# Kernel tuning notes

Hardware: AMD Instinct MI355X
Metric: run time of the kernel (lower is better)

The kernel has to match this reference:

```python
import jax, jax.numpy as jnp
import numpy as np

B_, T_, N_ = 32, 96, 68
IN_F, HID, GRU_H, NCLS = 3, 128, 128, 10
DEG = 8
N_NODES = B_ * T_ * N_
N_EDGES = N_NODES * DEG


def setup_inputs() -> dict:
    key = jax.random.key(0)
    ks = jax.random.split(key, 16)
    s = 0.05
    rn = lambda k, shp: (jax.random.normal(k, shp, jnp.float32) * s)
    return {
        "x": jax.random.normal(ks[0], (N_NODES, IN_F), jnp.float32),
        "edge_index": jax.random.randint(ks[1], (2, N_EDGES), 0, N_NODES, jnp.int32),
        "W_gcn0": rn(ks[2], (IN_F, HID)),
        "b_gcn0": jnp.zeros((HID,), jnp.float32),
        "W_gcn1": rn(ks[3], (HID, HID)),
        "b_gcn1": jnp.zeros((HID,), jnp.float32),
        "W_mlp": rn(ks[4], (HID, HID)),
        "b_mlp": jnp.zeros((HID,), jnp.float32),
        "W_ih": rn(ks[5], (3 * GRU_H, HID)),
        "W_hh": rn(ks[6], (3 * GRU_H, GRU_H)),
        "b_ih": jnp.zeros((3 * GRU_H,), jnp.float32),
        "b_hh": jnp.zeros((3 * GRU_H,), jnp.float32),
        "W_c1": rn(ks[7], (GRU_H, GRU_H // 2)),
        "b_c1": jnp.zeros((GRU_H // 2,), jnp.float32),
        "W_c2": rn(ks[8], (GRU_H // 2, NCLS)),
        "b_c2": jnp.zeros((NCLS,), jnp.float32),
        "B": B_, "T": T_, "N": N_,
    }


def reference(x, edge_index, W_gcn0, b_gcn0, W_gcn1, b_gcn1, W_mlp, b_mlp,
              W_ih, W_hh, b_ih, b_hh, W_c1, b_c1, W_c2, b_c2, B, T, N):
    n_nodes = x.shape[0]
    src, dst = edge_index[0], edge_index[1]
    # GCN degree with self-loops: deg[i] = 1 + in-degree(i)
    deg = jnp.ones((n_nodes,), x.dtype).at[dst].add(1.0)
    d_isqrt = jax.lax.rsqrt(deg)
    self_norm = (d_isqrt * d_isqrt)[:, None]  # self-loop norm = 1/deg
    edge_norm = (d_isqrt[src] * d_isqrt[dst])[:, None]

    def gcn(h, W, b):
        h = h @ W
        agg = jax.ops.segment_sum(h[src] * edge_norm, dst, num_segments=n_nodes)
        return agg + h * self_norm + b

    h = jax.nn.relu(gcn(x, W_gcn0, b_gcn0))
    h = jax.nn.relu(gcn(h, W_gcn1, b_gcn1))
    h = jax.nn.relu(h @ W_mlp + b_mlp)  # node_mlp (dropout off in eval)

    frames = h.reshape(B, T, N, -1).mean(axis=2)  # [B, T, HID] frame pooling

    def gru_step(hs, xt):
        gi = xt @ W_ih.T + b_ih
        gh = hs @ W_hh.T + b_hh
        ir, iz, inn = jnp.split(gi, 3, axis=-1)
        hr, hz, hn = jnp.split(gh, 3, axis=-1)
        r = jax.nn.sigmoid(ir + hr)
        z = jax.nn.sigmoid(iz + hz)
        n_new = jnp.tanh(inn + r * hn)
        return (1.0 - z) * n_new + z * hs, None

    h0 = jnp.zeros((B, GRU_H), frames.dtype)
    hT, _ = jax.lax.scan(gru_step, h0, jnp.swapaxes(frames, 0, 1))

    hidden = jax.nn.relu(hT @ W_c1 + b_c1)
    return hidden @ W_c2 + b_c2  # logits [B, num_classes]
```

## Files before the change

kernel.cpp:

```cpp
#include <hip/hip_runtime.h>

#define NN_TOT 208896
#define E_TOT  1671168
#define B_SZ   32
#define T_SZ   96
#define NPF    68
#define HID    128
#define NBINS  204
#define CAP    9216
#define NSB    816

typedef _Float16 f16x8 __attribute__((ext_vector_type(8)));
typedef _Float16 f16x2v __attribute__((ext_vector_type(2)));
typedef float f32x4 __attribute__((ext_vector_type(4)));

__global__ __launch_bounds__(256) void k_scatter(const int* __restrict__ src, const int* __restrict__ dst,
                                                 int* __restrict__ gcur, int* __restrict__ er_tmp,
                                                 const float* __restrict__ Wih, const float* __restrict__ Whh,
                                                 const float* __restrict__ W1, const float* __restrict__ Wm,
                                                 const float* __restrict__ W0, const float* __restrict__ b0,
                                                 _Float16* __restrict__ Wihh, _Float16* __restrict__ Wihl,
                                                 _Float16* __restrict__ W1p, _Float16* __restrict__ Wmp,
                                                 _Float16* __restrict__ Whhp, _Float16* __restrict__ W0h,
                                                 _Float16* __restrict__ b0h, float4* __restrict__ fr32v) {
    const int bid = blockIdx.x;
    const int tid = threadIdx.x;
    if (bid >= NSB) {
        int i = (bid - NSB) * 256 + tid;
        {
            const float4 z4 = make_float4(0.f, 0.f, 0.f, 0.f);
            fr32v[(size_t)i * 2] = z4;
            fr32v[(size_t)i * 2 + 1] = z4;
        }
        {
            int e = i & 7;
            int lane = (i >> 3) & 63;
            int f = i >> 9;
            int j = f >> 2, kk = f & 3;
            int q = lane >> 4, p = lane & 15;
            float wv = Wih[(size_t)(j * 16 + p) * 128 + kk * 32 + q * 8 + e];
            _Float16 hi = (_Float16)wv;
            Wihh[i] = hi;
            Wihl[i] = (_Float16)(wv - (float)hi);
        }
        {
            int e = i & 7;
            int lane = (i >> 3) & 63;
            int f = i >> 9;
            int kk = f & 3, g = (f >> 2) % 3, wv = f / 12;
            int q = lane >> 4, c = lane & 15;
            Whhp[i] = (_Float16)Whh[(size_t)(g * 128 + 16 * wv + c) * 128 + kk * 32 + q * 8 + e];
        }
        if (i < 16384) {
            int f = i >> 9;
            int j = f >> 2, kk = f & 3;
            int lane = (i >> 3) & 63;
            int e = i & 7;
            int q = lane >> 4, p = lane & 15;
            int k = kk * 32 + q * 8 + e, n = j * 16 + p;
            W1p[i] = (_Float16)W1[k * 128 + n];
            Wmp[i] = (_Float16)Wm[k * 128 + n];
        }
        if (i < 384) W0h[i] = (_Float16)W0[i];
        if (i < 128) b0h[i] = (_Float16)b0[i];
        return;
    }
    __shared__ int hist[NBINS];
    __shared__ int lofs[NBINS];
    __shared__ int lbase[NBINS];
    __shared__ int ts[256];
    __shared__ int recs[2048];
    __shared__ int dsta[2048];
    for (int i = tid; i < NBINS; i += 256) hist[i] = 0;
    __syncthreads();
    const int be = bid * 2048 + tid * 8;
    int s[8], d[8], rk[8];
    *(int4*)&s[0] = *(const int4*)&src[be];
    *(int4*)&s[4] = *(const int4*)&src[be + 4];
    *(int4*)&d[0] = *(const int4*)&dst[be];
    *(int4*)&d[4] = *(const int4*)&dst[be + 4];
#pragma unroll
    for (int j = 0; j < 8; ++j) rk[j] = atomicAdd(&hist[d[j] >> 10], 1);
    __syncthreads();
    {
        int v = (tid < NBINS) ? hist[tid] : 0;
        ts[tid] = v;
        __syncthreads();
        int inc = v;
        for (int off = 1; off < 256; off <<= 1) {
            int add = (tid >= off) ? ts[tid - off] : 0;
            __syncthreads();
            inc += add;
            ts[tid] = inc;
            __syncthreads();
        }
        if (tid < NBINS) lofs[tid] = inc - v;
    }
    for (int i = tid; i < NBINS; i += 256) lbase[i] = atomicAdd(&gcur[i], hist[i]);
    __syncthreads();
#pragma unroll
    for (int j = 0; j < 8; ++j) {
        int b = d[j] >> 10;
        int pos = lofs[b] + rk[j];
        recs[pos] = s[j] | ((d[j] & 1023) << 18);
        dsta[pos] = b * CAP + lbase[b] + rk[j];
    }
    __syncthreads();
#pragma unroll
    for (int it = 0; it < 8; ++it) {
        int p = tid + it * 256;
        er_tmp[dsta[p]] = recs[p];
    }
}

__global__ __launch_bounds__(256) void k_binsort2(const int* __restrict__ er_tmp, const int* __restrict__ gcur,
                                                  const float* __restrict__ x, int* __restrict__ er,
                                                  int2* __restrict__ row2, float4* __restrict__ xd) {
    __shared__ int lcnt[1024];
    __shared__ int lofs[1024];
    __shared__ int ts[256];
    const int tid = threadIdx.x;
    const int nb = blockIdx.x << 10;
    const int base0 = blockIdx.x * CAP;
    for (int i = tid; i < 1024; i += 256) lcnt[i] = 0;
    __syncthreads();
    const int nrec = gcur[blockIdx.x];
    int rec[36];
    int rnk[36];
#pragma unroll
    for (int j = 0; j < 36; ++j) {
        int idx = tid + j * 256;
        rec[j] = (idx < nrec) ? er_tmp[base0 + idx] : -1;
    }
#pragma unroll
    for (int j = 0; j < 36; ++j)
        rnk[j] = (rec[j] >= 0) ? atomicAdd(&lcnt[rec[j] >> 18], 1) : 0;
    __syncthreads();
    const int base = tid * 4;
    const int c0 = lcnt[base], c1 = lcnt[base + 1], c2 = lcnt[base + 2], c3 = lcnt[base + 3];
    int ssum = c0 + c1 + c2 + c3;
    ts[tid] = ssum;
    __syncthreads();
    int inc = ssum;
    for (int off = 1; off < 256; off <<= 1) {
        int add = (tid >= off) ? ts[tid - off] : 0;
        __syncthreads();
        inc += add;
        ts[tid] = inc;
        __syncthreads();
    }
    const int b0 = base0 + (inc - ssum);
    lofs[base] = b0;
    lofs[base + 1] = b0 + c0;
    lofs[base + 2] = b0 + c0 + c1;
    lofs[base + 3] = b0 + c0 + c1 + c2;
    row2[nb + base] = make_int2(b0, b0 + c0);
    row2[nb + base + 1] = make_int2(b0 + c0, b0 + c0 + c1);
    row2[nb + base + 2] = make_int2(b0 + c0 + c1, b0 + c0 + c1 + c2);
    row2[nb + base + 3] = make_int2(b0 + c0 + c1 + c2, b0 + ssum);
    {
        const float4* xv = (const float4*)(x + 3 * (size_t)(nb + base));
        float4 a = xv[0], b = xv[1], c = xv[2];
        float i0 = 1.0f / sqrtf(1.f + (float)c0);
        float i1 = 1.0f / sqrtf(1.f + (float)c1);
        float i2 = 1.0f / sqrtf(1.f + (float)c2);
        float i3 = 1.0f / sqrtf(1.f + (float)c3);
        xd[nb + base + 0] = make_float4(a.x * i0, a.y * i0, a.z * i0, i0);
        xd[nb + base + 1] = make_float4(a.w * i1, b.x * i1, b.y * i1, i1);
        xd[nb + base + 2] = make_float4(b.z * i2, b.w * i2, c.x * i2, i2);
        xd[nb + base + 3] = make_float4(c.y * i3, c.z * i3, c.w * i3, i3);
    }
    __syncthreads();
#pragma unroll
    for (int j = 0; j < 36; ++j)
        if (rec[j] >= 0) er[lofs[rec[j] >> 18] + rnk[j]] = rec[j] & 0x3FFFF;
}

__global__ __launch_bounds__(256) void k_z0(const float4* __restrict__ xd, const int2* __restrict__ row2,
                                            const int* __restrict__ er, float4* __restrict__ z0out) {
    const int tid = threadIdx.x;
    const int blk = blockIdx.x;
    const int li = tid >> 2;
    const int slot = tid & 3;
    const int n = blk * 64 + li;
    const int2 be2 = row2[n];
    float p0 = 0.f, p1 = 0.f, p2 = 0.f;
    for (int ei = be2.x + slot; ei < be2.y; ei += 4) {
        float4 f = xd[er[ei]];
        p0 += f.x;
        p1 += f.y;
        p2 += f.z;
    }
    p0 += __shfl_xor(p0, 1); p1 += __shfl_xor(p1, 1); p2 += __shfl_xor(p2, 1);
    p0 += __shfl_xor(p0, 2); p1 += __shfl_xor(p1, 2); p2 += __shfl_xor(p2, 2);
    if (slot == 0) {
        const float4 own = xd[n];
        const float w = own.w;
        float4 z;
        z.x = w * (p0 + own.x);
        z.y = w * (p1 + own.y);
        z.z = w * (p2 + own.z);
        z.w = w;
        z0out[n] = z;
    }
}

__global__ __launch_bounds__(256, 4) void k_agg_mm(const float4* __restrict__ z0, const int2* __restrict__ row2,
                                                   const int* __restrict__ er, const _Float16* __restrict__ W0h,
                                                   const _Float16* __restrict__ b0h, const _Float16* __restrict__ W1p,
                                                   const float* __restrict__ b1, const _Float16* __restrict__ Wmp,
                                                   const float* __restrict__ bm, float* __restrict__ fr32) {
    __shared__ __align__(16) _Float16 As[64 * 136];
    __shared__ __align__(16) _Float16 Bs[64 * 136];
    __shared__ float colpart[4 * 2 * 128];
    const int tid = threadIdx.x;
    const int w = tid >> 6, lane = tid & 63;
    const int blk = blockIdx.x;

    {
        const int node = blk * 64 + lane;
        const int2 be2 = row2[node];
        const int beg = be2.x, end = be2.y;
        int ei = beg;
        int sa_c = 0, sb_c = 0, sa_n = 0, sb_n = 0;
        float4 za_c, zb_c;
        if (ei + 2 <= end) { sa_c = er[ei]; sb_c = er[ei + 1]; }
        if (ei + 4 <= end) { sa_n = er[ei + 2]; sb_n = er[ei + 3]; }
        const float4 zs = z0[node];
        if (ei + 2 <= end) { za_c = z0[sa_c]; zb_c = z0[sb_c]; }

        const f16x2v* __restrict__ W0p = (const f16x2v*)W0h;
        const f16x2v* __restrict__ b0p = (const f16x2v*)b0h;
        const int pb = w * 16;
        const f16x2v zero2 = {(_Float16)0.f, (_Float16)0.f};
        f16x2v w0p[16], w1p[16], w2p[16], bbp[16];
#pragma unroll
        for (int j = 0; j < 16; ++j) {
            w0p[j] = W0p[pb + j];
            w1p[j] = W0p[64 + pb + j];
            w2p[j] = W0p[128 + pb + j];
            bbp[j] = b0p[pb + j];
        }
        const _Float16 isd = (_Float16)zs.w;
        const f16x2v dnn = {isd, isd};
        f16x2v accp[16];
        {
            _Float16 sx = (_Float16)zs.x, sy = (_Float16)zs.y, sz = (_Float16)zs.z;
            f16x2v zxx = {sx, sx}, zyy = {sy, sy}, zzz = {sz, sz};
#pragma unroll
            for (int j = 0; j < 16; ++j) {
                f16x2v t = zxx * w0p[j] + (zyy * w1p[j] + (zzz * w2p[j] + bbp[j]));
                t = __builtin_elementwise_max(t, zero2);
                accp[j] = t * dnn;
            }
        }
        for (; ei + 2 <= end; ei += 2) {
            float4 za_nv, zb_nv;
            int sa_nn = 0, sb_nn = 0;
            if (ei + 4 <= end) { za_nv = z0[sa_n]; zb_nv = z0[sb_n]; }
            if (ei + 6 <= end) { sa_nn = er[ei + 4]; sb_nn = er[ei + 5]; }
            const float4 za = za_c, zb = zb_c;
            _Float16 ax = (_Float16)za.x, ay = (_Float16)za.y, az = (_Float16)za.z;
            _Float16 aen = (_Float16)za.w;
            _Float16 bx = (_Float16)zb.x, by = (_Float16)zb.y, bz = (_Float16)zb.z;
            _Float16 ben = (_Float16)zb.w;
            f16x2v axx = {ax, ax}, ayy = {ay, ay}, azz = {az, az}, aee = {aen, aen};
            f16x2v bxx = {bx, bx}, byy = {by, by}, bzz = {bz, bz}, bee = {ben, ben};
#pragma unroll
            for (int j = 0; j < 16; ++j) {
                f16x2v t = axx * w0p[j] + (ayy * w1p[j] + (azz * w2p[j] + bbp[j]));
                t = __builtin_elementwise_max(t, zero2);
                accp[j] = t * aee + accp[j];
            }
#pragma unroll
            for (int j = 0; j < 16; ++j) {
                f16x2v t = bxx * w0p[j] + (byy * w1p[j] + (bzz * w2p[j] + bbp[j]));
                t = __builtin_elementwise_max(t, zero2);
                accp[j] = t * bee + accp[j];
            }
            za_c = za_nv; zb_c = zb_nv;
            sa_n = sa_nn; sb_n = sb_nn;
        }
        if (ei < end) {
            float4 za = z0[er[ei]];
            _Float16 ax = (_Float16)za.x, ay = (_Float16)za.y, az = (_Float16)za.z;
            _Float16 aen = (_Float16)za.w;
            f16x2v axx = {ax, ax}, ayy = {ay, ay}, azz = {az, az}, aee = {aen, aen};
#pragma unroll
            for (int j = 0; j < 16; ++j) {
                f16x2v t = axx * w0p[j] + (ayy * w1p[j] + (azz * w2p[j] + bbp[j]));
                t = __builtin_elementwise_max(t, zero2);
                accp[j] = t * aee + accp[j];
            }
        }
        _Float16* dst = &As[lane * 136 + w * 32];
#pragma unroll
        for (int j = 0; j < 16; ++j) *(f16x2v*)(dst + 2 * j) = accp[j] * dnn;
    }
    __syncthreads();

    const int q = lane >> 4, c = lane & 15;
    {
        f16x8 afr[4];
#pragma unroll
        for (int kk = 0; kk < 4; ++kk) afr[kk] = *(const f16x8*)(&As[(w * 16 + c) * 136 + kk * 32 + q * 8]);
        const f16x8* __restrict__ Bv = (const f16x8*)W1p;
#pragma unroll
        for (int j = 0; j < 8; ++j) {
            f32x4 cc = {0.f, 0.f, 0.f, 0.f};
#pragma unroll
            for (int kk = 0; kk < 4; ++kk)
                cc = __builtin_amdgcn_mfma_f32_16x16x32_f16(afr[kk], Bv[(j * 4 + kk) * 64 + lane], cc, 0, 0, 0);
            const float bi = b1[j * 16 + c];
#pragma unroll
            for (int r = 0; r < 4; ++r)
                Bs[(w * 16 + q * 4 + r) * 136 + j * 16 + c] = (_Float16)fmaxf(cc[r] + bi, 0.f);
        }
    }

    {
        f16x8 afr2[4];
#pragma unroll
        for (int kk = 0; kk < 4; ++kk) afr2[kk] = *(const f16x8*)(&Bs[(w * 16 + c) * 136 + kk * 32 + q * 8]);
        const f16x8* __restrict__ Bv2 = (const f16x8*)Wmp;
        const int f0 = (blk * 64) / NPF;
        const int cut = (f0 + 1) * NPF;
        const int rowg0 = blk * 64 + w * 16 + q * 4;
#pragma unroll
        for (int j = 0; j < 8; ++j) {
            f32x4 cc = {0.f, 0.f, 0.f, 0.f};
#pragma unroll
            for (int kk = 0; kk < 4; ++kk)
                cc = __builtin_amdgcn_mfma_f32_16x16x32_f16(afr2[kk], Bv2[(j * 4 + kk) * 64 + lane], cc, 0, 0, 0);
            const float bi = bm[j * 16 + c];
            float sA = 0.f, sB = 0.f;
#pragma unroll
            for (int r = 0; r < 4; ++r) {
                float v = fmaxf(cc[r] + bi, 0.f);
                if (rowg0 + r < cut) sA += v; else sB += v;
            }
            sA += __shfl_xor(sA, 16);
            sA += __shfl_xor(sA, 32);
            sB += __shfl_xor(sB, 16);
            sB += __shfl_xor(sB, 32);
            if (lane < 16) {
                colpart[(w * 2 + 0) * 128 + j * 16 + c] = sA;
                colpart[(w * 2 + 1) * 128 + j * 16 + c] = sB;
            }
        }
    }
    __syncthreads();
    {
        const int f = tid >> 7, col = tid & 127;
        float s = colpart[(0 * 2 + f) * 128 + col] + colpart[(1 * 2 + f) * 128 + col] +
                  colpart[(2 * 2 + f) * 128 + col] + colpart[(3 * 2 + f) * 128 + col];
        const int f0 = (blk * 64) / NPF;
        if (f == 0) {
            atomicAdd(&fr32[(size_t)f0 * 128 + col], s);
        } else {
            const int f1 = (blk * 64 + 63) / NPF;
            if (f1 != f0) atomicAdd(&fr32[(size_t)f1 * 128 + col], s);
        }
    }
}

__global__ __launch_bounds__(256) void k_gi(const float* __restrict__ fr32,
                                            const _Float16* __restrict__ Wihh, const _Float16* __restrict__ Wihl,
                                            const float* __restrict__ bih, const float* __restrict__ bhh,
                                            float* __restrict__ GIt) {
    __shared__ __align__(16) _Float16 Ah[64 * 136];
    __shared__ __align__(16) _Float16 Al[64 * 136];
    const int tid = threadIdx.x;
    const int w = tid >> 6, lane = tid & 63;
    const int q = lane >> 4, p = lane & 15;
    const int nb = blockIdx.x * 64;

    for (int idx = tid; idx < 64 * 128; idx += 256) {
        int row = idx >> 7, col = idx & 127;
        float v = fr32[(size_t)(nb + row) * 128 + col] * (1.0f / NPF);
        _Float16 hi = (_Float16)v;
        Ah[row * 136 + col] = hi;
        Al[row * 136 + col] = (_Float16)(v - (float)hi);
    }
    __syncthreads();

    f16x8 ah[4], al[4];
#pragma unroll
    for (int kk = 0; kk < 4; ++kk) {
        ah[kk] = *(const f16x8*)(&Ah[(w * 16 + p) * 136 + kk * 32 + q * 8]);
        al[kk] = *(const f16x8*)(&Al[(w * 16 + p) * 136 + kk * 32 + q * 8]);
    }
    const f16x8* __restrict__ Bh = (const f16x8*)Wihh;
    const f16x8* __restrict__ Bl = (const f16x8*)Wihl;
    int dr[4];
#pragma unroll
    for (int r = 0; r < 4; ++r) {
        int m = nb + w * 16 + q * 4 + r;
        int bb = m / 96, tt = m - bb * 96;
        dr[r] = (tt * B_SZ + bb) * 384;
    }
#pragma unroll
    for (int j = 0; j < 24; ++j) {
        f32x4 cc = {0.f, 0.f, 0.f, 0.f};
#pragma unroll
        for (int kk = 0; kk < 4; ++kk)
            cc = __builtin_amdgcn_mfma_f32_16x16x32_f16(ah[kk], Bh[(j * 4 + kk) * 64 + lane], cc, 0, 0, 0);
#pragma unroll
        for (int kk = 0; kk < 4; ++kk)
            cc = __builtin_amdgcn_mfma_f32_16x16x32_f16(ah[kk], Bl[(j * 4 + kk) * 64 + lane], cc, 0, 0, 0);
#pragma unroll
        for (int kk = 0; kk < 4; ++kk)
            cc = __builtin_amdgcn_mfma_f32_16x16x32_f16(al[kk], Bh[(j * 4 + kk) * 64 + lane], cc, 0, 0, 0);
        const int o = j * 16 + p;
        const float bias = bih[o] + ((o < 256) ? bhh[o] : 0.f);
        const float scale = (o < 256) ? -1.44269504f : 1.f;
#pragma unroll
        for (int r = 0; r < 4; ++r) GIt[dr[r] + o] = (cc[r] + bias) * scale;
    }
}

#define GRU_SYNC()                                              \
    asm volatile("s_waitcnt lgkmcnt(0)" ::: "memory");          \
    __builtin_amdgcn_s_barrier();                               \
    __builtin_amdgcn_sched_barrier(0);

#define GRU_BODY(PAR, GU, GL, JOFF)                                                                  \
    {                                                                                                \
        const _Float16* rb = hbuf[PAR];                                                              \
        _Float16* wb = hbuf[PAR ^ 1];                                                                \
        f16x8 afr[4];                                                                                \
        _Pragma("unroll") for (int kk = 0; kk < 4; ++kk)                                             \
            afr[kk] = *(const f16x8*)(&rb[c * 144 + kk * 32 + q * 8]);                               \
        const float* lp = pb + (size_t)(JOFF + 2) * STRIDE;                                          \
        _Pragma("unroll") for (int r = 0; r < 4; ++r)                                                \
            _Pragma("unroll") for (int g = 0; g < 3; ++g)                                            \
                GL[r * 3 + g] = lp[r * 384 + g * 128];                                               \
        f32x4 cc[3];                                                                                 \
        _Pragma("unroll") for (int g = 0; g < 3; ++g) {                                              \
            f32x4 a = {0.f, 0.f, 0.f, 0.f};                                                          \
            _Pragma("unroll") for (int kk = 0; kk < 4; ++kk)                                         \
                a = __builtin_amdgcn_mfma_f32_16x16x32_f16(afr[kk], bfr[g][kk], a, 0, 0, 0);         \
            cc[g] = a;                                                                               \
        }                                                                                            \
        _Pragma("unroll") for (int r = 0; r < 4; ++r) {                                              \
            float hn = cc[2][r] + bh2;                                                               \
            float rg = __builtin_amdgcn_rcpf(1.f + exp2f(fmaf(mL2E, cc[0][r], GU[r * 3 + 0])));      \
            float zg = __builtin_amdgcn_rcpf(1.f + exp2f(fmaf(mL2E, cc[1][r], GU[r * 3 + 1])));      \
            float arg = fmaf(rg, hn, GU[r * 3 + 2]);                                                 \
            float u = __builtin_amdgcn_rcpf(exp2f(2.f * L2E * arg) + 1.f);                           \
            float nn = fmaf(-2.f, u, 1.f);                                                           \
            h[r] = fmaf(zg, h[r] - nn, nn);                                                          \
            if (q < 2) wb[(q * 4 + r) * 144 + 16 * w + c] = (_Float16)h[r];                          \
        }                                                                                            \
        GRU_SYNC()                                                                                   \
    }

__global__ __launch_bounds__(512) __attribute__((amdgpu_waves_per_eu(1, 2)))
void k_gru(const float* __restrict__ GIt, const _Float16* __restrict__ Whhp,
           const float* __restrict__ bhh,
           const float* __restrict__ Wc1, const float* __restrict__ bc1,
           const float* __restrict__ Wc2, const float* __restrict__ bc2,
           float* __restrict__ out) {
    __shared__ __align__(16) _Float16 hbuf[2][16 * 144];
    const int tid = threadIdx.x;
    const int w = tid >> 6, lane = tid & 63;
    const int q = lane >> 4, c = lane & 15;
    const int B = blockIdx.x;
    const float L2E = 1.44269504f;
    const float mL2E = -1.44269504f;
    const int STRIDE = B_SZ * 384;

    f16x8 bfr[3][4];
#pragma unroll
    for (int g = 0; g < 3; ++g)
#pragma unroll
        for (int kk = 0; kk < 4; ++kk)
            bfr[g][kk] = *(const f16x8*)(Whhp + (size_t)(((w * 3 + g) * 4 + kk) * 64 + lane) * 8);
    const float bh2 = bhh[256 + 16 * w + c];
    for (int i = tid; i < 2 * 16 * 144 / 2; i += 512) ((unsigned int*)hbuf)[i] = 0u;
    float h[4] = {0.f, 0.f, 0.f, 0.f};

    const int qq = (q < 2) ? q : 1;
    const float* pb = GIt + (size_t)(B * 8 + qq * 4) * 384 + 16 * w + c;
    float g0[12], g1[12], g2[12];
#pragma unroll
    for (int r = 0; r < 4; ++r)
#pragma unroll
        for (int g = 0; g < 3; ++g) {
            g0[r * 3 + g] = pb[r * 384 + g * 128];
            g1[r * 3 + g] = pb[STRIDE + r * 384 + g * 128];
        }
    GRU_SYNC()

    for (int it = 0; it < T_SZ / 6; ++it) {
        GRU_BODY(0, g0, g2, 0)
        GRU_BODY(1, g1, g0, 1)
        GRU_BODY(0, g2, g1, 2)
        GRU_BODY(1, g0, g2, 3)
        GRU_BODY(0, g1, g0, 4)
        GRU_BODY(1, g2, g1, 5)
        pb += 6 * (size_t)STRIDE;
    }

    float* hbf = (float*)hbuf;
    float* hid = hbf + 1024;
    __syncthreads();
    if (q < 2) {
#pragma unroll
        for (int r = 0; r < 4; ++r) hbf[(q * 4 + r) * 128 + 16 * w + c] = h[r];
    }
    __syncthreads();
    {
        const int b = tid >> 6, j = tid & 63;
        const float* hb = hbf + b * 128;
        float a0 = bc1[j], a1 = 0.f, a2 = 0.f, a3 = 0.f;
#pragma unroll
        for (int k = 0; k < 128; k += 4) {
            a0 = fmaf(hb[k], Wc1[k * 64 + j], a0);
            a1 = fmaf(hb[k + 1], Wc1[(k + 1) * 64 + j], a1);
            a2 = fmaf(hb[k + 2], Wc1[(k + 2) * 64 + j], a2);
            a3 = fmaf(hb[k + 3], Wc1[(k + 3) * 64 + j], a3);
        }
        hid[tid] = fmaxf((a0 + a1) + (a2 + a3), 0.f);
    }
    __syncthreads();
    if (tid < 80) {
        int b = tid / 10, cc2 = tid % 10;
        float a = bc2[cc2];
#pragma unroll 8
        for (int k = 0; k < 64; ++k) a = fmaf(hid[b * 64 + k], Wc2[k * 10 + cc2], a);
        out[(B * 8 + b) * 10 + cc2] = a;
    }
}

extern "C" void kernel_launch(void* const* d_in, const int* in_sizes, int n_in, void* d_out, int out_size, void* d_ws,
                              size_t ws_size, hipStream_t stream) {
    const float* x = (const float*)d_in[0];
    const int* ei = (const int*)d_in[1];
    const int* e_src = ei;
    const int* e_dst = ei + E_TOT;
    const float* W0 = (const float*)d_in[2];
    const float* b0 = (const float*)d_in[3];
    const float* W1 = (const float*)d_in[4];
    const float* b1 = (const float*)d_in[5];
    const float* Wm = (const float*)d_in[6];
    const float* bm = (const float*)d_in[7];
    const float* Wih = (const float*)d_in[8];
    const float* Whh = (const float*)d_in[9];
    const float* bih = (const float*)d_in[10];
    const float* bhh = (const float*)d_in[11];
    const float* Wc1 = (const float*)d_in[12];
    const float* bc1 = (const float*)d_in[13];
    const float* Wc2 = (const float*)d_in[14];
    const float* bc2 = (const float*)d_in[15];
    float* out = (float*)d_out;

    char* base = (char*)d_ws;
    size_t off = 0;
    auto alloc = [&](size_t bytes) {
        size_t o = off;
        off = (off + bytes + 255) & ~(size_t)255;
        return o;
    };
    size_t o_gcur = alloc(256 * 4);
    size_t o_row2 = alloc((size_t)NN_TOT * 8);
    size_t o_er = alloc((size_t)NBINS * CAP * 4);
    size_t o_ertmp = alloc((size_t)NBINS * CAP * 4);
    size_t o_xd = alloc((size_t)NN_TOT * 16);
    size_t o_fr32 = alloc((size_t)B_SZ * T_SZ * 128 * 4);
    size_t o_gi = alloc((size_t)(T_SZ + 2) * B_SZ * 384 * 4);
    size_t o_wihh = alloc((size_t)384 * 128 * 2);
    size_t o_wihl = alloc((size_t)384 * 128 * 2);
    size_t o_w1p = alloc((size_t)128 * 128 * 2);
    size_t o_wmp = alloc((size_t)128 * 128 * 2);
    size_t o_whhp = alloc((size_t)128 * 384 * 2);
    size_t o_w0h = alloc((size_t)384 * 2);
    size_t o_b0h = alloc((size_t)128 * 2);
    size_t o_z0 = alloc((size_t)NN_TOT * 16);
    if (off > ws_size) return;

    int* gcur = (int*)(base + o_gcur);
    int2* row2 = (int2*)(base + o_row2);
    int* er = (int*)(base + o_er);
    int* er_tmp = (int*)(base + o_ertmp);
    float4* xd = (float4*)(base + o_xd);
    float* fr32 = (float*)(base + o_fr32);
    float* GIt = (float*)(base + o_gi);
    _Float16* Wihh = (_Float16*)(base + o_wihh);
    _Float16* Wihl = (_Float16*)(base + o_wihl);
    _Float16* W1p = (_Float16*)(base + o_w1p);
    _Float16* Wmp = (_Float16*)(base + o_wmp);
    _Float16* Whhp = (_Float16*)(base + o_whhp);
    _Float16* W0h = (_Float16*)(base + o_w0h);
    _Float16* b0h = (_Float16*)(base + o_b0h);
    float4* z0 = (float4*)(base + o_z0);

    hipMemsetAsync(base + o_gcur, 0, 256 * 4, stream);

    k_scatter<<<NSB + 192, 256, 0, stream>>>(e_src, e_dst, gcur, er_tmp,
                                             Wih, Whh, W1, Wm, W0, b0,
                                             Wihh, Wihl, W1p, Wmp, Whhp, W0h, b0h, (float4*)fr32);
    k_binsort2<<<NBINS, 256, 0, stream>>>(er_tmp, gcur, x, er, row2, xd);
    k_z0<<<NN_TOT / 64, 256, 0, stream>>>(xd, row2, er, z0);
    k_agg_mm<<<NN_TOT / 64, 256, 0, stream>>>(z0, row2, er, W0h, b0h, W1p, b1, Wmp, bm, fr32);
    k_gi<<<B_SZ * T_SZ / 64, 256, 0, stream>>>(fr32, Wihh, Wihl, bih, bhh, GIt);
    k_gru<<<4, 512, 0, stream>>>(GIt, Whhp, bhh, Wc1, bc1, Wc2, bc2, out);
}
```

Measured before the change: 338.3 us.

## Split GRU across eight blocks of four batch rows with shuffle-compacted gates

The GRU recurrence kernel now runs eight blocks of four batch rows each, instead of four blocks of eight. After each step's MFMA, the valid output rows are moved with lane shuffles so that every lane computes exactly one gate element. Before, each lane computed four row elements, half of them padding. This cuts the per-step sigmoid/tanh and global-load work on the serial critical path and spreads the recurrence over more CUs. The cost is extra cross-lane shuffles and select logic in every step, and the MFMA tiles now use only a quarter of their rows.

```diff
diff --git a/kernel.cpp b/kernel.cpp
--- a/kernel.cpp
+++ b/kernel.cpp
@@ -432,9 +432,7 @@
         _Pragma("unroll") for (int kk = 0; kk < 4; ++kk)                                             \
             afr[kk] = *(const f16x8*)(&rb[c * 144 + kk * 32 + q * 8]);                               \
         const float* lp = pb + (size_t)(JOFF + 2) * STRIDE;                                          \
-        _Pragma("unroll") for (int r = 0; r < 4; ++r)                                                \
-            _Pragma("unroll") for (int g = 0; g < 3; ++g)                                            \
-                GL[r * 3 + g] = lp[r * 384 + g * 128];                                               \
+        _Pragma("unroll") for (int g = 0; g < 3; ++g) GL[g] = lp[g * 128];                           \
         f32x4 cc[3];                                                                                 \
         _Pragma("unroll") for (int g = 0; g < 3; ++g) {                                              \
             f32x4 a = {0.f, 0.f, 0.f, 0.f};                                                          \
@@ -442,15 +440,23 @@
                 a = __builtin_amdgcn_mfma_f32_16x16x32_f16(afr[kk], bfr[g][kk], a, 0, 0, 0);         \
             cc[g] = a;                                                                               \
         }                                                                                            \
-        _Pragma("unroll") for (int r = 0; r < 4; ++r) {                                              \
-            float hn = cc[2][r] + bh2;                                                               \
-            float rg = __builtin_amdgcn_rcpf(1.f + exp2f(fmaf(mL2E, cc[0][r], GU[r * 3 + 0])));      \
-            float zg = __builtin_amdgcn_rcpf(1.f + exp2f(fmaf(mL2E, cc[1][r], GU[r * 3 + 1])));      \
-            float arg = fmaf(rg, hn, GU[r * 3 + 2]);                                                 \
+        float sg[3];                                                                                 \
+        _Pragma("unroll") for (int g = 0; g < 3; ++g) {                                              \
+            float x0 = __shfl(cc[g][0], c);                                                          \
+            float x1 = __shfl(cc[g][1], c);                                                          \
+            float x2 = __shfl(cc[g][2], c);                                                          \
+            float x3 = __shfl(cc[g][3], c);                                                          \
+            sg[g] = (q == 0) ? x0 : (q == 1) ? x1 : (q == 2) ? x2 : x3;                              \
+        }                                                                                            \
+        {                                                                                            \
+            float hn = sg[2] + bh2;                                                                  \
+            float rg = __builtin_amdgcn_rcpf(1.f + exp2f(fmaf(mL2E, sg[0], GU[0])));                 \
+            float zg = __builtin_amdgcn_rcpf(1.f + exp2f(fmaf(mL2E, sg[1], GU[1])));                 \
+            float arg = fmaf(rg, hn, GU[2]);                                                         \
             float u = __builtin_amdgcn_rcpf(exp2f(2.f * L2E * arg) + 1.f);                           \
             float nn = fmaf(-2.f, u, 1.f);                                                           \
-            h[r] = fmaf(zg, h[r] - nn, nn);                                                          \
-            if (q < 2) wb[(q * 4 + r) * 144 + 16 * w + c] = (_Float16)h[r];                          \
+            h = fmaf(zg, h - nn, nn);                                                                \
+            wb[q * 144 + gcol] = (_Float16)h;                                                        \
         }                                                                                            \
         GRU_SYNC()                                                                                   \
     }
@@ -476,20 +482,18 @@
 #pragma unroll
         for (int kk = 0; kk < 4; ++kk)
             bfr[g][kk] = *(const f16x8*)(Whhp + (size_t)(((w * 3 + g) * 4 + kk) * 64 + lane) * 8);
-    const float bh2 = bhh[256 + 16 * w + c];
+    const int gcol = w * 16 + c;
+    const float bh2 = bhh[256 + gcol];
     for (int i = tid; i < 2 * 16 * 144 / 2; i += 512) ((unsigned int*)hbuf)[i] = 0u;
-    float h[4] = {0.f, 0.f, 0.f, 0.f};
-
-    const int qq = (q < 2) ? q : 1;
-    const float* pb = GIt + (size_t)(B * 8 + qq * 4) * 384 + 16 * w + c;
-    float g0[12], g1[12], g2[12];
-#pragma unroll
-    for (int r = 0; r < 4; ++r)
-#pragma unroll
-        for (int g = 0; g < 3; ++g) {
-            g0[r * 3 + g] = pb[r * 384 + g * 128];
-            g1[r * 3 + g] = pb[STRIDE + r * 384 + g * 128];
-        }
+    float h = 0.f;
+
+    const float* pb = GIt + (size_t)(B * 4 + q) * 384 + gcol;
+    float g0[3], g1[3], g2[3];
+#pragma unroll
+    for (int g = 0; g < 3; ++g) {
+        g0[g] = pb[g * 128];
+        g1[g] = pb[STRIDE + g * 128];
+    }
     GRU_SYNC()
 
     for (int it = 0; it < T_SZ / 6; ++it) {
@@ -503,14 +507,11 @@
     }
 
     float* hbf = (float*)hbuf;
-    float* hid = hbf + 1024;
-    __syncthreads();
-    if (q < 2) {
-#pragma unroll
-        for (int r = 0; r < 4; ++r) hbf[(q * 4 + r) * 128 + 16 * w + c] = h[r];
-    }
-    __syncthreads();
-    {
+    float* hid = hbf + 512;
+    __syncthreads();
+    hbf[q * 128 + gcol] = h;
+    __syncthreads();
+    if (tid < 256) {
         const int b = tid >> 6, j = tid & 63;
         const float* hb = hbf + b * 128;
         float a0 = bc1[j], a1 = 0.f, a2 = 0.f, a3 = 0.f;
@@ -524,12 +525,12 @@
         hid[tid] = fmaxf((a0 + a1) + (a2 + a3), 0.f);
     }
     __syncthreads();
-    if (tid < 80) {
+    if (tid < 40) {
         int b = tid / 10, cc2 = tid % 10;
         float a = bc2[cc2];
 #pragma unroll 8
         for (int k = 0; k < 64; ++k) a = fmaf(hid[b * 64 + k], Wc2[k * 10 + cc2], a);
-        out[(B * 8 + b) * 10 + cc2] = a;
+        out[(B * 4 + b) * 10 + cc2] = a;
     }
 }
 
@@ -604,5 +605,5 @@
     k_z0<<<NN_TOT / 64, 256, 0, stream>>>(xd, row2, er, z0);
     k_agg_mm<<<NN_TOT / 64, 256, 0, stream>>>(z0, row2, er, W0h, b0h, W1p, b1, Wmp, bm, fr32);
     k_gi<<<B_SZ * T_SZ / 64, 256, 0, stream>>>(fr32, Wihh, Wihl, bih, bhh, GIt);
-    k_gru<<<4, 512, 0, stream>>>(GIt, Whhp, bhh, Wc1, bc1, Wc2, bc2, out);
+    k_gru<<<8, 512, 0, stream>>>(GIt, Whhp, bhh, Wc1, bc1, Wc2, bc2, out);
 }
```

Measured after the change: 310.2 us. 8.3% less time.
